# Kernel optimization log

Hardware: AMD Instinct MI355X
Metric: run time of the kernel (lower is better)

## Reference

```python
import jax, jax.numpy as jnp
import numpy as np

B, S, E, H, VS, VT = 128, 256, 512, 512, 32000, 32000


def _lstm_layer(x, mask, Wih, Whh, bih, bhh):
    # x: (S,B,E_in), mask: (S,B) bool. PyTorch gate order i,f,g,o.
    h0 = jnp.zeros((x.shape[1], Whh.shape[1]), x.dtype)
    c0 = h0
    def step(carry, inp):
        h, c = carry
        xt, mt = inp
        g = xt @ Wih.T + h @ Whh.T + bih + bhh
        i, f, gg, o = jnp.split(g, 4, axis=-1)
        i = jax.nn.sigmoid(i); f = jax.nn.sigmoid(f)
        gg = jnp.tanh(gg); o = jax.nn.sigmoid(o)
        c_new = f * c + i * gg
        h_new = o * jnp.tanh(c_new)
        m = mt[:, None]
        h2 = jnp.where(m, h_new, h)
        c2 = jnp.where(m, c_new, c)
        return (h2, c2), jnp.where(m, h_new, 0.0)  # pad_packed zero-pads
    (hT, cT), ys = jax.lax.scan(step, (h0, c0), (x, mask))
    return ys, cT


def setup_inputs() -> dict:
    key = jax.random.key(0)
    ks = jax.random.split(key, 32)
    def w(k, shape, fan_in):
        bound = 1.0 / np.sqrt(fan_in)
        return jax.random.uniform(k, shape, jnp.float32, -bound, bound)
    src_tokens = jax.random.randint(ks[0], (B, S), 0, VS)
    src_lens = jnp.sort(jax.random.randint(ks[1], (B,), S // 2, S + 1))[::-1]
    src_lens = src_lens.at[0].set(S)  # pack_padded expects descending, max = S
    trg_tokens = jax.random.randint(ks[2], (B,), 0, VT)
    inp = {
        'src_tokens': src_tokens, 'src_lens': src_lens, 'trg_tokens': trg_tokens,
        'src_emb': jax.random.normal(ks[3], (VS, E), jnp.float32),
        'trg_emb': jax.random.normal(ks[4], (VT, E), jnp.float32),
        'enc_Wih0': w(ks[5], (4 * H, E), H), 'enc_Whh0': w(ks[6], (4 * H, H), H),
        'enc_bih0': w(ks[7], (4 * H,), H), 'enc_bhh0': w(ks[8], (4 * H,), H),
        'enc_Wih1': w(ks[9], (4 * H, H), H), 'enc_Whh1': w(ks[10], (4 * H, H), H),
        'enc_bih1': w(ks[11], (4 * H,), H), 'enc_bhh1': w(ks[12], (4 * H,), H),
        'dec_Wih': w(ks[13], (4 * H, E + H), H), 'dec_Whh': w(ks[14], (4 * H, H), H),
        'dec_bih': w(ks[15], (4 * H,), H), 'dec_bhh': w(ks[16], (4 * H,), H),
        'W_init': w(ks[17], (H, 2 * H), 2 * H), 'b_init': w(ks[18], (H,), 2 * H),
        'W_hid': w(ks[19], (H, 2 * H), 2 * H), 'b_hid': w(ks[20], (H,), 2 * H),
        'W_out': w(ks[21], (VT, H), H), 'b_out': w(ks[22], (VT,), H),
    }
    return inp


def reference(src_tokens, src_lens, trg_tokens, src_emb, trg_emb,
              enc_Wih0, enc_Whh0, enc_bih0, enc_bhh0,
              enc_Wih1, enc_Whh1, enc_bih1, enc_bhh1,
              dec_Wih, dec_Whh, dec_bih, dec_bhh,
              W_init, b_init, W_hid, b_hid, W_out, b_out):
    # ---- encode ----
    x = src_emb[src_tokens]                       # (B,S,E)
    x = jnp.transpose(x, (1, 0, 2))               # (S,B,E)
    mask = jnp.arange(S)[:, None] < src_lens[None, :]  # (S,B)
    y0, c0f = _lstm_layer(x, mask, enc_Wih0, enc_Whh0, enc_bih0, enc_bhh0)
    y1, c1f = _lstm_layer(y0, mask, enc_Wih1, enc_Whh1, enc_bih1, enc_bhh1)
    src_states = jnp.transpose(y1, (1, 0, 2))     # (B,S,H)
    # final cell states (num_layers,B,H) -> (B, num_layers*H)
    final_cells = jnp.concatenate([c0f, c1f], axis=-1)  # (B,2H)
    c_dec = final_cells @ W_init.T + b_init       # (B,H)
    h_dec = jnp.tanh(c_dec)
    # ---- one decoder step ----
    emb_t = trg_emb[trg_tokens]                   # (B,E)
    vec = jnp.concatenate([emb_t, jnp.zeros((B, H), emb_t.dtype)], axis=-1)
    g = vec @ dec_Wih.T + h_dec @ dec_Whh.T + dec_bih + dec_bhh
    i, f, gg, o = jnp.split(g, 4, axis=-1)
    c = jax.nn.sigmoid(f) * c_dec + jax.nn.sigmoid(i) * jnp.tanh(gg)
    h = jax.nn.sigmoid(o) * jnp.tanh(c)           # (B,H)
    # ---- masked dot attention ----
    scores = jnp.einsum('bsh,bh->bs', src_states, h)
    smask = jnp.arange(S)[None, :] < src_lens[:, None]
    scores = jnp.where(smask, scores, -jnp.inf)
    attw = jax.nn.softmax(scores, axis=-1)
    context = jnp.einsum('bs,bsh->bh', attw, src_states)
    attn_vec = jnp.concatenate([h, context], axis=-1) @ W_hid.T + b_hid
    logits = attn_vec @ W_out.T + b_out
    prd_token = jnp.argmax(logits, axis=-1)       # softmax is monotone
    return context, h, prd_token
```

## Files before the change

### kernel.cpp

```cpp
#include <hip/hip_runtime.h>
#include <stdint.h>


typedef _Float16 f16;
typedef f16 f16x8 __attribute__((ext_vector_type(8)));
typedef float f32x4 __attribute__((ext_vector_type(4)));

#define LOSCALE 2048.0f
#define LOINV   (1.0f/2048.0f)

#define B_  128
#define S_  256
#define H_  512

__device__ __forceinline__ uint16_t hbits(f16 h){ union{ f16 f; uint16_t u; } c; c.f=h; return c.u; }

__device__ __forceinline__ uint32_t split_ph2(float x){
  f16 h = (f16)x;
  float r = (x - (float)h) * LOSCALE;
  return (uint32_t)hbits(h) | ((uint32_t)hbits((f16)r) << 16);
}
__device__ __forceinline__ float ph2val(uint32_t p){
  union{ uint16_t u; f16 f; } a, b; a.u = (uint16_t)p; b.u = (uint16_t)(p>>16);
  return (float)a.f + (float)b.f * LOINV;
}

__device__ __forceinline__ void pack_hi_lo(const uint4& a, const uint4& b, uint4& hi, uint4& lo){
  hi = make_uint4((a.x & 0xffffu) | (a.y << 16),
                  (a.z & 0xffffu) | (a.w << 16),
                  (b.x & 0xffffu) | (b.y << 16),
                  (b.z & 0xffffu) | (b.w << 16));
  lo = make_uint4((a.x >> 16) | (a.y & 0xffff0000u),
                  (a.z >> 16) | (a.w & 0xffff0000u),
                  (b.x >> 16) | (b.y & 0xffff0000u),
                  (b.z >> 16) | (b.w & 0xffff0000u));
}

__device__ __forceinline__ void split_pack8(const float* x, uint4& hi, uint4& lo){
  uint16_t h[8], l[8];
#pragma unroll
  for (int e = 0; e < 8; ++e) {
    f16 hh = (f16)x[e];
    float r = (x[e] - (float)hh) * LOSCALE;
    h[e] = hbits(hh); l[e] = hbits((f16)r);
  }
  hi = make_uint4((uint32_t)h[0]|((uint32_t)h[1]<<16), (uint32_t)h[2]|((uint32_t)h[3]<<16),
                  (uint32_t)h[4]|((uint32_t)h[5]<<16), (uint32_t)h[6]|((uint32_t)h[7]<<16));
  lo = make_uint4((uint32_t)l[0]|((uint32_t)l[1]<<16), (uint32_t)l[2]|((uint32_t)l[3]<<16),
                  (uint32_t)l[4]|((uint32_t)l[5]<<16), (uint32_t)l[6]|((uint32_t)l[7]<<16));
}

__device__ __forceinline__ f32x4 mfma16(uint4 a, uint4 b, f32x4 c){
  return __builtin_amdgcn_mfma_f32_16x16x32_f16(
      __builtin_bit_cast(f16x8, a), __builtin_bit_cast(f16x8, b), c, 0, 0, 0);
}

__device__ __forceinline__ float sigm(float x){ return 1.0f/(1.0f + expf(-x)); }
__device__ __forceinline__ float fsigm(float x){ return 1.0f/(1.0f + __expf(-x)); }
__device__ __forceinline__ float ftanh(float x){
  float ax = fabsf(x);
  float e = __expf(-2.0f*ax);
  float r = (1.0f - e)/(1.0f + e);
  return copysignf(r, x);
}

__device__ __forceinline__ uint32_t plane_word(uint32_t p, uint32_t pp, int odd){
  return odd ? ((pp >> 16) | (p & 0xffff0000u))
             : ((p & 0xffffu) | (pp << 16));
}

__device__ __forceinline__ size_t fl_idx(int row, int k){
  return (size_t)(k >> 5) * 4096 + (size_t)(row >> 4) * 512 + (size_t)(k & 1) * 256
       + (size_t)((k >> 3) & 3) * 64 + (size_t)(row & 15) * 4 + (size_t)((k & 7) >> 1);
}

__device__ __forceinline__ void gload_lds16(const uint32_t* gbase, uint32_t* lbase, int lane){
#if __has_builtin(__builtin_amdgcn_global_load_lds)
  __builtin_amdgcn_global_load_lds(
      (const __attribute__((address_space(1))) uint32_t*)(gbase + lane*4),
      (__attribute__((address_space(3))) uint32_t*)lbase, 16, 0, 0);
#else
  *(uint4*)(lbase + lane*4) = *(const uint4*)(gbase + lane*4);
#endif
}

__global__ __launch_bounds__(256) void k_embed_src_fl(const int* __restrict__ tok,
    const float* __restrict__ emb, uint32_t* __restrict__ out)
{
  const size_t total = (size_t)S_ * B_ * H_;
  for (size_t i = (size_t)blockIdx.x*256 + threadIdx.x; i < total; i += (size_t)gridDim.x*256) {
    int s = (int)(i >> 16), b = (int)((i >> 9) & 127), k = (int)(i & 511);
    int t = tok[b*S_ + s];
    uint32_t p = split_ph2(emb[(size_t)t*H_ + k]);
    uint32_t pp = __shfl_xor(p, 1);
    out[(size_t)s*65536 + fl_idx(b, k)] = plane_word(p, pp, k & 1);
  }
}

__global__ __launch_bounds__(256) void k_embed_trg(const int* __restrict__ tok,
    const float* __restrict__ emb, uint32_t* __restrict__ out)
{
  int i = blockIdx.x*256 + threadIdx.x;
  int e = i & (H_-1), b = i >> 9;
  int t = tok[b];
  out[i] = split_ph2(emb[(size_t)t*H_ + e]);
}

__global__ __launch_bounds__(256) void k_packW(const float* __restrict__ W,
    uint32_t* __restrict__ out)
{
  int i = blockIdx.x*256 + threadIdx.x;
  int n = i >> 9, k = i & 511;
  uint32_t p = split_ph2(W[i]);
  uint32_t pp = __shfl_xor(p, 1);
  out[(size_t)(n >> 7)*65536 + fl_idx(n & 127, k)] = plane_word(p, pp, k & 1);
}

__global__ __launch_bounds__(256) void k_packAfl(const float* __restrict__ a,
    uint32_t* __restrict__ out)
{
  int i = blockIdx.x*256 + threadIdx.x;
  int b = i >> 9, k = i & 511;
  uint32_t p = split_ph2(a[i]);
  uint32_t pp = __shfl_xor(p, 1);
  out[fl_idx(b, k)] = plane_word(p, pp, k & 1);
}

__global__ __launch_bounds__(256,2) void k_gemm_fl(
    const uint32_t* __restrict__ Afl,
    const uint32_t* __restrict__ Wfl,
    const float* __restrict__ b0, const float* __restrict__ b1,
    float* __restrict__ C, int N, int addC)
{
  __shared__ uint8_t sm[65536];
  const int tid = threadIdx.x, lane = tid & 63, wv = tid >> 6;
  const int wm = wv >> 1, wn = wv & 1;
  const int bn0 = blockIdx.x * 128, bm0 = blockIdx.y * 128;
  const uint32_t* Ab = Afl + (size_t)blockIdx.y * 65536;
  const uint32_t* Wb = Wfl + (size_t)blockIdx.x * 65536;

  f32x4 acc0[4][4], acc1[4][4];
#pragma unroll
  for (int i = 0; i < 4; ++i)
#pragma unroll
    for (int j = 0; j < 4; ++j) { acc0[i][j] = (f32x4){0,0,0,0}; acc1[i][j] = (f32x4){0,0,0,0}; }

  for (int it = 0; it < 8; ++it) {
    __syncthreads();
    {
      const uint32_t* gsrc = (wv < 2 ? Ab : Wb) + (size_t)it*8192 + (size_t)(wv & 1)*4096;
      uint32_t* lb = (uint32_t*)(sm + (size_t)wv*16384);
#pragma unroll
      for (int e = 0; e < 16; ++e)
        gload_lds16(gsrc + e*256, lb + e*256, lane);
    }
    asm volatile("s_waitcnt vmcnt(0)" ::: "memory");
    __syncthreads();

#pragma unroll
    for (int kt = 0; kt < 2; ++kt) {
      uint4 ah[4], al[4];
#pragma unroll
      for (int i = 0; i < 4; ++i) {
        const uint8_t* p = sm + (size_t)(kt*8 + wm*4 + i)*2048 + lane*16;
        ah[i] = *(const uint4*)p; al[i] = *(const uint4*)(p + 1024);
      }
#pragma unroll
      for (int j = 0; j < 4; ++j) {
        const uint8_t* p = sm + 32768 + (size_t)(kt*8 + wn*4 + j)*2048 + lane*16;
        uint4 bh = *(const uint4*)p;
        uint4 bl = *(const uint4*)(p + 1024);
#pragma unroll
        for (int i = 0; i < 4; ++i) {
          acc0[i][j] = mfma16(ah[i], bh, acc0[i][j]);
          acc1[i][j] = mfma16(al[i], bh, acc1[i][j]);
          acc1[i][j] = mfma16(ah[i], bl, acc1[i][j]);
        }
      }
    }
  }

#pragma unroll
  for (int i = 0; i < 4; ++i) {
    int row0 = bm0 + (wm*4+i)*16 + ((lane>>4)<<2);
#pragma unroll
    for (int j = 0; j < 4; ++j) {
      int col = bn0 + (wn*4+j)*16 + (lane & 15);
      float bias = 0.f;
      if (b0) bias += b0[col];
      if (b1) bias += b1[col];
      f32x4 v = acc0[i][j] + acc1[i][j] * LOINV;
#pragma unroll
      for (int r = 0; r < 4; ++r) {
        size_t idx = (size_t)(row0 + r) * N + col;
        float out = v[r] + bias;
        if (addC) out += C[idx];
        C[idx] = out;
      }
    }
  }
}

__global__ __launch_bounds__(256,2) void k_gemm(
    const uint32_t* __restrict__ A, int lda,
    const float* __restrict__ W, int ldw,
    const float* __restrict__ b0, const float* __restrict__ b1,
    float* __restrict__ C, int N, int K, int addC)
{
  __shared__ uint8_t sm[65536];
  const int tid = threadIdx.x;
  const int lane = tid & 63, wv = tid >> 6;
  const int wm = wv >> 1, wn = wv & 1;
  const int bn0 = blockIdx.x * 128, bm0 = blockIdx.y * 128;

  const int srow = tid >> 1;
  const int skh  = (tid & 1) * 32;
  const int smt  = srow >> 4, sr = srow & 15, skt = tid & 1;

  f32x4 acc0[4][4], acc1[4][4];
#pragma unroll
  for (int i = 0; i < 4; ++i)
#pragma unroll
    for (int j = 0; j < 4; ++j) { acc0[i][j] = (f32x4){0,0,0,0}; acc1[i][j] = (f32x4){0,0,0,0}; }

  for (int k0 = 0; k0 < K; k0 += 64) {
    __syncthreads();
    {
      const uint32_t* ap = A + (size_t)(bm0 + srow) * lda + (k0 + skh);
      uint4 q[8];
#pragma unroll
      for (int e = 0; e < 8; ++e) q[e] = *(const uint4*)(ap + e*4);
#pragma unroll
      for (int kg = 0; kg < 4; ++kg) {
        uint4 hi, lo; pack_hi_lo(q[2*kg], q[2*kg+1], hi, lo);
        uint8_t* dst = sm + (size_t)(smt*2 + skt)*2048 + (size_t)(sr + 16*kg)*16;
        *(uint4*)dst = hi; *(uint4*)(dst + 1024) = lo;
      }
    }
    {
      const float* wp = W + (size_t)(bn0 + srow) * ldw + (k0 + skh);
      float xs[32];
#pragma unroll
      for (int e = 0; e < 8; ++e) { float4 v = *(const float4*)(wp + e*4);
        xs[e*4+0]=v.x; xs[e*4+1]=v.y; xs[e*4+2]=v.z; xs[e*4+3]=v.w; }
#pragma unroll
      for (int kg = 0; kg < 4; ++kg) {
        uint4 hi, lo; split_pack8(xs + kg*8, hi, lo);
        uint8_t* dst = sm + 32768 + (size_t)(smt*2 + skt)*2048 + (size_t)(sr + 16*kg)*16;
        *(uint4*)dst = hi; *(uint4*)(dst + 1024) = lo;
      }
    }
    __syncthreads();

#pragma unroll
    for (int kt = 0; kt < 2; ++kt) {
      uint4 ah[4], al[4];
#pragma unroll
      for (int i = 0; i < 4; ++i) {
        const uint8_t* p = sm + (size_t)(((wm*4+i)*2 + kt))*2048 + lane*16;
        ah[i] = *(const uint4*)p; al[i] = *(const uint4*)(p + 1024);
      }
#pragma unroll
      for (int j = 0; j < 4; ++j) {
        const uint8_t* p = sm + 32768 + (size_t)(((wn*4+j)*2 + kt))*2048 + lane*16;
        uint4 bh = *(const uint4*)p;
        uint4 bl = *(const uint4*)(p + 1024);
#pragma unroll
        for (int i = 0; i < 4; ++i) {
          acc0[i][j] = mfma16(ah[i], bh, acc0[i][j]);
          acc1[i][j] = mfma16(al[i], bh, acc1[i][j]);
          acc1[i][j] = mfma16(ah[i], bl, acc1[i][j]);
        }
      }
    }
  }

#pragma unroll
  for (int i = 0; i < 4; ++i) {
    int row0 = bm0 + (wm*4+i)*16 + ((lane>>4)<<2);
#pragma unroll
    for (int j = 0; j < 4; ++j) {
      int col = bn0 + (wn*4+j)*16 + (lane & 15);
      float bias = 0.f;
      if (b0) bias += b0[col];
      if (b1) bias += b1[col];
      f32x4 v = acc0[i][j] + acc1[i][j] * LOINV;
#pragma unroll
      for (int r = 0; r < 4; ++r) {
        size_t idx = (size_t)(row0 + r) * N + col;
        float out = v[r] + bias;
        if (addC) out += C[idx];
        C[idx] = out;
      }
    }
  }
}

__global__ __launch_bounds__(256,1) void k_lstm2(
    const float* __restrict__ Whh0, const float* __restrict__ Whh1,
    const float* __restrict__ bih1, const float* __restrict__ bhh1,
    const float* __restrict__ xg,
    const int*  __restrict__ lens,
    uint32_t* __restrict__ mb0,
    uint32_t* __restrict__ mb1,
    float* __restrict__ cb0, float* __restrict__ cb1,
    uint32_t* __restrict__ y1buf,
    uint32_t* __restrict__ flg0, uint32_t* __restrict__ flg1,
    const uint32_t* __restrict__ Wp1,
    int s0, int nt)
{
  __shared__ uint8_t sm[163840];
  uint8_t* wih = sm;
  uint8_t* tile = sm + 131072;
  uint64_t* tile64 = (uint64_t*)tile;
  float* g0ex = (float*)tile;
  float* g1ex = (float*)(tile + 4096);

  const int tid = threadIdx.x, lane = tid & 63, wv = tid >> 6;
  const int bg = blockIdx.x & 7, hs = blockIdx.x >> 3;
  const int row = lane & 15, qh = lane >> 4;

  {
    const uint32_t* wpb = Wp1 + (size_t)(wv*4 + (hs >> 3))*65536 + (size_t)(hs & 7)*512;
    uint32_t* lb = (uint32_t*)(wih + (size_t)wv*32768);
#pragma unroll
    for (int kt = 0; kt < 16; ++kt) {
      gload_lds16(wpb + kt*4096,       lb + kt*512,       lane);
      gload_lds16(wpb + kt*4096 + 256, lb + kt*512 + 256, lane);
    }
  }

  uint4 w0h[16], w0l[16], w1h[16], w1l[16];
  {
    const float* r0 = Whh0 + (size_t)(wv*512 + hs*16 + row)*512 + qh*8;
    const float* r1 = Whh1 + (size_t)(wv*512 + hs*16 + row)*512 + qh*8;
#pragma unroll
    for (int kt = 0; kt < 16; ++kt) {
      float xs[8];
      float4 v0 = *(const float4*)(r0 + kt*32), v1 = *(const float4*)(r0 + kt*32 + 4);
      xs[0]=v0.x; xs[1]=v0.y; xs[2]=v0.z; xs[3]=v0.w;
      xs[4]=v1.x; xs[5]=v1.y; xs[6]=v1.z; xs[7]=v1.w;
      split_pack8(xs, w0h[kt], w0l[kt]);
      v0 = *(const float4*)(r1 + kt*32); v1 = *(const float4*)(r1 + kt*32 + 4);
      xs[0]=v0.x; xs[1]=v0.y; xs[2]=v0.z; xs[3]=v0.w;
      xs[4]=v1.x; xs[5]=v1.y; xs[6]=v1.z; xs[7]=v1.w;
      split_pack8(xs, w1h[kt], w1l[kt]);
    }
  }

  const int b_l = tid >> 4, uu = tid & 15;
  const int bglob = bg*16 + b_l;
  const size_t bgoff = (size_t)bg*8192;
  const int oct_p = hs*2 + (uu >> 3);
  const size_t widx = (size_t)b_l*512 + (size_t)(uu & 1)*256
                    + ((size_t)(oct_p ^ b_l) << 2) + (size_t)((uu & 7) >> 1);
  const int len_b = lens[bglob];
  const int lenA  = lens[bg*16 + row];
  float c0_reg = cb0[(size_t)bglob*512 + hs*16 + uu];
  float c1_reg = cb1[(size_t)bglob*512 + hs*16 + uu];
  float h0_reg, h1_reg;
  {
    size_t ib = (size_t)(s0 & 1)*65536 + bgoff + (size_t)b_l*512
              + ((size_t)(oct_p ^ b_l) << 2) + (size_t)((uu & 7) >> 1);
    uint32_t hiw = mb0[ib], low = mb0[ib + 256];
    int sh = (uu & 1) * 16;
    union{ uint16_t u; f16 f; } ch, cl;
    ch.u = (uint16_t)(hiw >> sh); cl.u = (uint16_t)(low >> sh);
    h0_reg = (float)ch.f + (float)cl.f * LOINV;
    int s1i = (s0 >= 1) ? (s0 - 1) : 0;
    size_t ib1 = (size_t)(s1i & 1)*65536 + bgoff + (size_t)b_l*512
               + ((size_t)(oct_p ^ b_l) << 2) + (size_t)((uu & 7) >> 1);
    hiw = mb1[ib1]; low = mb1[ib1 + 256];
    ch.u = (uint16_t)(hiw >> sh); cl.u = (uint16_t)(low >> sh);
    h1_reg = (float)ch.f + (float)cl.f * LOINV;
  }
  float b1g[4];
#pragma unroll
  for (int g = 0; g < 4; ++g)
    b1g[g] = bih1[g*512 + hs*16 + uu] + bhh1[g*512 + hs*16 + uu];
  const size_t yfl = (size_t)(hs >> 1)*4096 + (size_t)bg*512 + (size_t)(uu & 1)*256
                   + (size_t)((((hs & 1) << 1) | (uu >> 3)))*64 + (size_t)b_l*4
                   + (size_t)((uu & 7) >> 1);

  asm volatile("s_waitcnt vmcnt(0)" ::: "memory");
  __syncthreads();

  for (int it = 0; it < nt; ++it) {
    const int t = s0 + it;
    const bool aL0 = (t < 256);
    const bool aL1 = (t > 0);

    float xv0 = 0.f, xv1 = 0.f, xv2 = 0.f, xv3 = 0.f;
    if (aL0) {
      const float* xgp = xg + ((size_t)it*128 + bglob)*2048 + hs*16 + uu;
      xv0 = xgp[0]; xv1 = xgp[512]; xv2 = xgp[1024]; xv3 = xgp[1536];
    }

    if (it > 0) {
      if (wv == 0) {
        const uint32_t* fp = flg0 + bg*32 + (lane & 31);
        while (1) {
          uint32_t f = __hip_atomic_load(fp, __ATOMIC_RELAXED, __HIP_MEMORY_SCOPE_SYSTEM);
          if (__all((int)(f >= (uint32_t)t))) break;
          __builtin_amdgcn_s_sleep(1);
        }
      } else if (wv == 1) {
        const uint32_t* fp = flg1 + bg*32 + (lane & 31);
        while (1) {
          uint32_t f = __hip_atomic_load(fp, __ATOMIC_RELAXED, __HIP_MEMORY_SCOPE_SYSTEM);
          if (__all((int)(f >= (uint32_t)(t - 1)))) break;
          __builtin_amdgcn_s_sleep(1);
        }
      }
    }
    __builtin_amdgcn_s_barrier();
    __builtin_amdgcn_sched_barrier(0);

    const uint64_t* sp0 = (const uint64_t*)(mb0 + (size_t)(t & 1)*65536 + bgoff);
    const uint64_t* sp1 = (const uint64_t*)(mb1 + (size_t)((t - 1) & 1)*65536 + bgoff);
    uint64_t v0[16], v1[16];
#pragma unroll
    for (int e = 0; e < 16; ++e)
      v0[e] = __hip_atomic_load(sp0 + tid + e*256, __ATOMIC_RELAXED, __HIP_MEMORY_SCOPE_SYSTEM);
    if (aL1) {
#pragma unroll
      for (int e = 0; e < 16; ++e)
        v1[e] = __hip_atomic_load(sp1 + tid + e*256, __ATOMIC_RELAXED, __HIP_MEMORY_SCOPE_SYSTEM);
    }
#pragma unroll
    for (int e = 0; e < 16; ++e)
      tile64[tid + e*256] = v0[e];
    asm volatile("s_waitcnt lgkmcnt(0)" ::: "memory");
    __builtin_amdgcn_s_barrier();
    __builtin_amdgcn_sched_barrier(0);

    f32x4 A0 = (f32x4){0,0,0,0}, A1 = (f32x4){0,0,0,0}, A2 = (f32x4){0,0,0,0};
    f32x4 B0 = (f32x4){0,0,0,0}, B1 = (f32x4){0,0,0,0}, B2 = (f32x4){0,0,0,0};
    {
      const uint8_t* hrp = tile + (size_t)row*2048;
      const uint8_t* wbase = wih + (size_t)wv*32768;
      const bool cY = aL1 && ((t - 1) < lenA);
      const uint4 z4 = make_uint4(0,0,0,0);
#pragma unroll
      for (int kt = 0; kt < 16; ++kt) {
        int oct = kt*4 + qh;
        const uint8_t* pA = hrp + (((oct ^ row)) << 4);
        uint4 ah = *(const uint4*)pA, al = *(const uint4*)(pA + 1024);
        A0 = mfma16(ah, w0h[kt], A0);
        A1 = mfma16(al, w0h[kt], A1);
        A2 = mfma16(ah, w0l[kt], A2);
        uint4 yh = cY ? ah : z4, yl = cY ? al : z4;
        const uint8_t* pB = wbase + (size_t)kt*2048 + lane*16;
        uint4 bh = *(const uint4*)pB, bl = *(const uint4*)(pB + 1024);
        B0 = mfma16(yh, bh, B0);
        B1 = mfma16(yl, bh, B1);
        B2 = mfma16(yh, bl, B2);
      }
    }
    __builtin_amdgcn_sched_barrier(0);
    __builtin_amdgcn_s_barrier();
    __builtin_amdgcn_sched_barrier(0);

    if (aL1) {
#pragma unroll
      for (int e = 0; e < 16; ++e)
        tile64[tid + e*256] = v1[e];
    }
    asm volatile("s_waitcnt lgkmcnt(0)" ::: "memory");
    __builtin_amdgcn_s_barrier();
    __builtin_amdgcn_sched_barrier(0);

    if (aL1) {
      const uint8_t* hrp = tile + (size_t)row*2048;
#pragma unroll
      for (int kt = 0; kt < 16; ++kt) {
        int oct = kt*4 + qh;
        const uint8_t* pA = hrp + (((oct ^ row)) << 4);
        uint4 ah = *(const uint4*)pA, al = *(const uint4*)(pA + 1024);
        B0 = mfma16(ah, w1h[kt], B0);
        B1 = mfma16(al, w1h[kt], B1);
        B2 = mfma16(ah, w1l[kt], B2);
      }
    }
    __builtin_amdgcn_sched_barrier(0);
    __builtin_amdgcn_s_barrier();
    __builtin_amdgcn_sched_barrier(0);

    {
      int col = lane & 15, rb = (lane >> 4) << 2;
      if (aL0) {
#pragma unroll
        for (int r = 0; r < 4; ++r)
          g0ex[(size_t)(wv*16 + rb + r)*16 + col] = A0[r] + (A1[r] + A2[r])*LOINV;
      }
      if (aL1) {
#pragma unroll
        for (int r = 0; r < 4; ++r)
          g1ex[(size_t)(wv*16 + rb + r)*16 + col] = B0[r] + (B1[r] + B2[r])*LOINV;
      }
    }
    asm volatile("s_waitcnt lgkmcnt(0)" ::: "memory");
    __builtin_amdgcn_s_barrier();
    __builtin_amdgcn_sched_barrier(0);

    uint32_t p1w = 0; bool m1 = false;
    if (aL0) {
      float gi = g0ex[(size_t)(0*16 + b_l)*16 + uu] + xv0;
      float gf = g0ex[(size_t)(1*16 + b_l)*16 + uu] + xv1;
      float gg = g0ex[(size_t)(2*16 + b_l)*16 + uu] + xv2;
      float go = g0ex[(size_t)(3*16 + b_l)*16 + uu] + xv3;
      float cn = fsigm(gf)*c0_reg + fsigm(gi)*ftanh(gg);
      float hn = fsigm(go)*ftanh(cn);
      bool m = (t < len_b);
      c0_reg = m ? cn : c0_reg;
      h0_reg = m ? hn : h0_reg;
      uint32_t p = split_ph2(h0_reg);
      uint32_t pp = __shfl_xor(p, 1);
      __hip_atomic_store(mb0 + (size_t)((t + 1) & 1)*65536 + bgoff + widx,
                         plane_word(p, pp, uu & 1), __ATOMIC_RELAXED, __HIP_MEMORY_SCOPE_SYSTEM);
    }
    if (aL1) {
      float gi = g1ex[(size_t)(0*16 + b_l)*16 + uu] + b1g[0];
      float gf = g1ex[(size_t)(1*16 + b_l)*16 + uu] + b1g[1];
      float gg = g1ex[(size_t)(2*16 + b_l)*16 + uu] + b1g[2];
      float go = g1ex[(size_t)(3*16 + b_l)*16 + uu] + b1g[3];
      float cn = fsigm(gf)*c1_reg + fsigm(gi)*ftanh(gg);
      float hn = fsigm(go)*ftanh(cn);
      m1 = ((t - 1) < len_b);
      c1_reg = m1 ? cn : c1_reg;
      h1_reg = m1 ? hn : h1_reg;
      uint32_t p = split_ph2(h1_reg);
      uint32_t pp = __shfl_xor(p, 1);
      p1w = plane_word(p, pp, uu & 1);
      __hip_atomic_store(mb1 + (size_t)(t & 1)*65536 + bgoff + widx,
                         p1w, __ATOMIC_RELAXED, __HIP_MEMORY_SCOPE_SYSTEM);
    }
    asm volatile("s_waitcnt vmcnt(0)" ::: "memory");
    __builtin_amdgcn_s_barrier();
    __builtin_amdgcn_sched_barrier(0);
    if (tid == 0) {
      if (aL0) __hip_atomic_store(flg0 + bg*32 + hs, (uint32_t)(t + 1),
                                  __ATOMIC_RELAXED, __HIP_MEMORY_SCOPE_SYSTEM);
      if (aL1) __hip_atomic_store(flg1 + bg*32 + hs, (uint32_t)t,
                                  __ATOMIC_RELAXED, __HIP_MEMORY_SCOPE_SYSTEM);
    }
    if (aL1) y1buf[(size_t)(t - 1)*65536 + yfl] = m1 ? p1w : 0u;
  }
  cb0[(size_t)bglob*512 + hs*16 + uu] = c0_reg;
  cb1[(size_t)bglob*512 + hs*16 + uu] = c1_reg;
}

__global__ __launch_bounds__(256) void k_pack2(const float* __restrict__ a,
    const float* __restrict__ b, uint32_t* __restrict__ out)
{
  int i = blockIdx.x*256 + threadIdx.x;
  int bb = i >> 10, k = i & 1023;
  float x = (k < 512) ? a[(size_t)bb*512 + k] : b[(size_t)bb*512 + k - 512];
  out[i] = split_ph2(x);
}

__global__ __launch_bounds__(256) void k_tanh_split(const float* __restrict__ c,
    uint32_t* __restrict__ hp)
{ int i = blockIdx.x*256 + threadIdx.x; hp[i] = split_ph2(tanhf(c[i])); }

__global__ __launch_bounds__(256) void k_dec_cell(const float* __restrict__ g,
    const float* __restrict__ cdec, float* __restrict__ hout, float* __restrict__ dh)
{
  int i = blockIdx.x*256 + threadIdx.x;
  int b = i >> 9, u = i & 511;
  const float* gb = g + (size_t)b*2048;
  float c = sigm(gb[512 + u])*cdec[i] + sigm(gb[u])*tanhf(gb[1024 + u]);
  float h = sigm(gb[1536 + u])*tanhf(c);
  hout[i] = h; dh[i] = h;
}

__global__ __launch_bounds__(256) void k_attn(const uint32_t* __restrict__ y1,
    const float* __restrict__ h, const int* __restrict__ lens,
    float* __restrict__ ctx, float* __restrict__ dctx)
{
  __shared__ float hsh[512];
  __shared__ float sc[256];
  __shared__ float red[8];
  const int b = blockIdx.x, tid = threadIdx.x, lane = tid & 63, wv = tid >> 6;
  hsh[tid]       = h[(size_t)b*512 + tid];
  hsh[tid + 256] = h[(size_t)b*512 + tid + 256];
  const int len = lens[b];
  __syncthreads();

  const size_t lanebase = (size_t)(lane >> 2)*4096 + (size_t)(b >> 4)*512
                        + (size_t)(lane & 3)*64 + (size_t)(b & 15)*4;
  for (int it = 0; it < 64; ++it) {
    int s = wv*64 + it;
    const uint32_t* yb = y1 + (size_t)s*65536 + lanebase;
    uint4 hw = *(const uint4*)yb;
    uint4 lw = *(const uint4*)(yb + 256);
    int k0 = lane*8;
    uint32_t hws[4] = {hw.x,hw.y,hw.z,hw.w}, lws[4] = {lw.x,lw.y,lw.z,lw.w};
    float d = 0.f;
#pragma unroll
    for (int w = 0; w < 4; ++w) {
      union{uint16_t u; f16 f;} h0,h1,l0,l1;
      h0.u=(uint16_t)hws[w]; h1.u=(uint16_t)(hws[w]>>16);
      l0.u=(uint16_t)lws[w]; l1.u=(uint16_t)(lws[w]>>16);
      d += ((float)h0.f + (float)l0.f*LOINV) * hsh[k0 + 2*w]
         + ((float)h1.f + (float)l1.f*LOINV) * hsh[k0 + 2*w + 1];
    }
    for (int off = 32; off; off >>= 1) d += __shfl_xor(d, off);
    if (lane == 0) sc[s] = d;
  }
  __syncthreads();

  float v = (tid < len) ? sc[tid] : -INFINITY;
  float mx = v;
  for (int off = 32; off; off >>= 1) mx = fmaxf(mx, __shfl_xor(mx, off));
  if (lane == 0) red[wv] = mx;
  __syncthreads();
  mx = fmaxf(fmaxf(red[0], red[1]), fmaxf(red[2], red[3]));
  float e = (tid < len) ? expf(v - mx) : 0.f;
  float ssum = e;
  for (int off = 32; off; off >>= 1) ssum += __shfl_xor(ssum, off);
  if (lane == 0) red[4 + wv] = ssum;
  __syncthreads();
  float tot = red[4] + red[5] + red[6] + red[7];
  __syncthreads();
  sc[tid] = e / tot;
  __syncthreads();

  const int u0 = tid, u1 = tid + 256;
  const size_t bu0 = (size_t)(u0 >> 5)*4096 + (size_t)(b >> 4)*512
                   + (size_t)((u0 >> 3) & 3)*64 + (size_t)(b & 15)*4 + (size_t)((u0 & 7) >> 1);
  const size_t bu1 = (size_t)(u1 >> 5)*4096 + (size_t)(b >> 4)*512
                   + (size_t)((u1 >> 3) & 3)*64 + (size_t)(b & 15)*4 + (size_t)((u1 & 7) >> 1);
  const int sh = (tid & 1) * 16;
  float acc0 = 0.f, acc1 = 0.f;
  for (int s = 0; s < 256; ++s) {
    float w = sc[s];
    const uint32_t* yb = y1 + (size_t)s*65536;
    uint32_t hi0 = yb[bu0], lo0 = yb[bu0 + 256];
    uint32_t hi1 = yb[bu1], lo1 = yb[bu1 + 256];
    union{uint16_t u; f16 f;} a,b2,c2,d2;
    a.u =(uint16_t)(hi0 >> sh); b2.u=(uint16_t)(lo0 >> sh);
    c2.u=(uint16_t)(hi1 >> sh); d2.u=(uint16_t)(lo1 >> sh);
    acc0 += w*((float)a.f  + (float)b2.f*LOINV);
    acc1 += w*((float)c2.f + (float)d2.f*LOINV);
  }
  ctx [(size_t)b*512 + tid]       = acc0;  ctx [(size_t)b*512 + tid + 256] = acc1;
  dctx[(size_t)b*512 + tid]       = acc0;  dctx[(size_t)b*512 + tid + 256] = acc1;
}

__global__ __launch_bounds__(256) void k_argmax(const float* __restrict__ logits,
    float* __restrict__ out)
{
  __shared__ float bv[256];
  __shared__ int   bi[256];
  const int b = blockIdx.x, tid = threadIdx.x;
  const float* L = logits + (size_t)b*32000;
  float best = -INFINITY; int idx = 0;
  for (int i = tid; i < 32000; i += 256) {
    float v = L[i];
    if (v > best) { best = v; idx = i; }
  }
  bv[tid] = best; bi[tid] = idx;
  __syncthreads();
  for (int sft = 128; sft; sft >>= 1) {
    if (tid < sft) {
      if (bv[tid+sft] > bv[tid] || (bv[tid+sft] == bv[tid] && bi[tid+sft] < bi[tid])) {
        bv[tid] = bv[tid+sft]; bi[tid] = bi[tid+sft];
      }
    }
    __syncthreads();
  }
  if (tid == 0) out[b] = (float)bi[0];
}

extern "C" void kernel_launch(void* const* d_in, const int* in_sizes, int n_in,
                              void* d_out, int out_size, void* d_ws, size_t ws_size,
                              hipStream_t stream)
{
  (void)in_sizes; (void)n_in; (void)out_size; (void)ws_size;
  const int*   src_tokens = (const int*)  d_in[0];
  const int*   src_lens   = (const int*)  d_in[1];
  const int*   trg_tokens = (const int*)  d_in[2];
  const float* src_emb    = (const float*)d_in[3];
  const float* trg_emb    = (const float*)d_in[4];
  const float* Wih0 = (const float*)d_in[5];
  const float* Whh0 = (const float*)d_in[6];
  const float* bih0 = (const float*)d_in[7];
  const float* bhh0 = (const float*)d_in[8];
  const float* Wih1 = (const float*)d_in[9];
  const float* Whh1 = (const float*)d_in[10];
  const float* bih1 = (const float*)d_in[11];
  const float* bhh1 = (const float*)d_in[12];
  const float* dWih = (const float*)d_in[13];
  const float* dWhh = (const float*)d_in[14];
  const float* dbih = (const float*)d_in[15];
  const float* dbhh = (const float*)d_in[16];
  const float* Winit= (const float*)d_in[17];
  const float* binit= (const float*)d_in[18];
  const float* Whid = (const float*)d_in[19];
  const float* bhid = (const float*)d_in[20];
  const float* Wout = (const float*)d_in[21];
  const float* bout = (const float*)d_in[22];

  uint8_t* ws = (uint8_t*)d_ws;
  constexpr size_t MBs = 1ull << 20;
  constexpr size_t OFF_AP    = 0;
  constexpr size_t OFF_Y1    = 64*MBs;
  constexpr size_t OFF_XG    = 128*MBs;
  constexpr size_t OFF_MB    = 192*MBs;
  constexpr size_t OFF_CB0   = OFF_MB    + 1*MBs;
  constexpr size_t OFF_CB1   = OFF_CB0   + 256*1024;
  constexpr size_t OFF_FLG   = OFF_CB1   + 256*1024;
  constexpr size_t OFF_PK    = OFF_FLG   + 4096;
  constexpr size_t OFF_CDEC  = OFF_PK    + 512*1024;
  constexpr size_t OFF_HDECP = OFF_CDEC  + 256*1024;
  constexpr size_t OFF_EMBP  = OFF_HDECP + 256*1024;
  constexpr size_t OFF_G     = OFF_EMBP  + 256*1024;
  constexpr size_t OFF_HDEC2 = OFF_G     + 1*MBs;
  constexpr size_t OFF_CTX   = OFF_HDEC2 + 256*1024;
  constexpr size_t OFF_AVEC  = OFF_CTX   + 256*1024;
  constexpr size_t OFF_AVECP = OFF_AVEC  + 256*1024;
  constexpr size_t OFF_LOG   = OFF_AVECP + 256*1024;

  uint32_t* Ap    = (uint32_t*)(ws + OFF_AP);
  uint32_t* Y1    = (uint32_t*)(ws + OFF_Y1);
  float*    Xg    = (float*)   (ws + OFF_XG);
  uint32_t* WoutF = (uint32_t*)(ws + OFF_XG);
  uint32_t* mb0   = (uint32_t*)(ws + OFF_MB);
  uint32_t* mb1   = (uint32_t*)(ws + OFF_MB + 512*1024);
  float*    cb0   = (float*)   (ws + OFF_CB0);
  float*    cb1   = (float*)   (ws + OFF_CB1);
  uint32_t* flg0  = (uint32_t*)(ws + OFF_FLG);
  uint32_t* flg1  = (uint32_t*)(ws + OFF_FLG + 2048);
  uint32_t* pk    = (uint32_t*)(ws + OFF_PK);
  float*    cdec  = (float*)   (ws + OFF_CDEC);
  uint32_t* hdecp = (uint32_t*)(ws + OFF_HDECP);
  uint32_t* embp  = (uint32_t*)(ws + OFF_EMBP);
  float*    g     = (float*)   (ws + OFF_G);
  float*    hdec2 = (float*)   (ws + OFF_HDEC2);
  float*    ctx   = (float*)   (ws + OFF_CTX);
  float*    avec  = (float*)   (ws + OFF_AVEC);
  uint32_t* avecp = (uint32_t*)(ws + OFF_AVECP);
  float*    logit = (float*)   (ws + OFF_LOG);
  uint32_t* Wp0   = (uint32_t*)(ws + OFF_LOG);
  uint32_t* Wp1   = (uint32_t*)(ws + OFF_LOG + 4*MBs);
  float*    dout  = (float*)   d_out;

  k_packW<<<4096, 256, 0, stream>>>(Wih0, Wp0);
  k_packW<<<4096, 256, 0, stream>>>(Wih1, Wp1);

  hipMemsetAsync(mb0,  0, 1024*1024, stream);
  hipMemsetAsync(flg0, 0, 4096, stream);
  hipMemsetAsync(cb0,  0, 65536*4, stream);
  hipMemsetAsync(cb1,  0, 65536*4, stream);
  k_embed_src_fl<<<2048, 256, 0, stream>>>(src_tokens, src_emb, Ap);
  for (int c = 0; c < 4; ++c) {
    int s0 = c * 64;
    k_gemm_fl<<<dim3(16, 64), 256, 0, stream>>>(Ap + (size_t)s0*65536,
        Wp0, bih0, bhh0, Xg, 2048, 0);
    k_lstm2<<<256, 256, 0, stream>>>(Whh0, Whh1, bih1, bhh1, Xg, src_lens,
        mb0, mb1, cb0, cb1, Y1, flg0, flg1, Wp1, s0, (c == 3) ? 65 : 64);
  }

  k_packW<<<64000, 256, 0, stream>>>(Wout, WoutF);

  k_pack2<<<512, 256, 0, stream>>>(cb0, cb1, pk);
  k_gemm<<<dim3(4, 1), 256, 0, stream>>>(pk, 1024, Winit, 1024, binit, nullptr,
      cdec, 512, 1024, 0);
  k_tanh_split<<<256, 256, 0, stream>>>(cdec, hdecp);

  k_embed_trg<<<256, 256, 0, stream>>>(trg_tokens, trg_emb, embp);
  k_gemm<<<dim3(16, 1), 256, 0, stream>>>(embp, 512, dWih, 1024, dbih, dbhh,
      g, 2048, 512, 0);
  k_gemm<<<dim3(16, 1), 256, 0, stream>>>(hdecp, 512, dWhh, 512, nullptr, nullptr,
      g, 2048, 512, 1);
  k_dec_cell<<<256, 256, 0, stream>>>(g, cdec, hdec2, dout + 65536);

  k_attn<<<128, 256, 0, stream>>>(Y1, hdec2, src_lens, ctx, dout);

  k_pack2<<<512, 256, 0, stream>>>(hdec2, ctx, pk);
  k_gemm<<<dim3(4, 1), 256, 0, stream>>>(pk, 1024, Whid, 1024, bhid, nullptr,
      avec, 512, 1024, 0);
  k_packAfl<<<256, 256, 0, stream>>>(avec, avecp);
  k_gemm_fl<<<dim3(250, 1), 256, 0, stream>>>(avecp, WoutF, bout, nullptr,
      logit, 32000, 0);
  k_argmax<<<128, 256, 0, stream>>>(logit, dout + 131072);
}
```

Before: 2.484 ms.

## Split fused two-layer LSTM step into separately synchronized layer phases

```diff
diff --git a/kernel.cpp b/kernel.cpp
--- a/kernel.cpp
+++ b/kernel.cpp
@@ -396,47 +396,34 @@
       xv0 = xgp[0]; xv1 = xgp[512]; xv2 = xgp[1024]; xv3 = xgp[1536];
     }
 
-    if (it > 0) {
-      if (wv == 0) {
-        const uint32_t* fp = flg0 + bg*32 + (lane & 31);
-        while (1) {
-          uint32_t f = __hip_atomic_load(fp, __ATOMIC_RELAXED, __HIP_MEMORY_SCOPE_SYSTEM);
-          if (__all((int)(f >= (uint32_t)t))) break;
-          __builtin_amdgcn_s_sleep(1);
-        }
-      } else if (wv == 1) {
-        const uint32_t* fp = flg1 + bg*32 + (lane & 31);
-        while (1) {
-          uint32_t f = __hip_atomic_load(fp, __ATOMIC_RELAXED, __HIP_MEMORY_SCOPE_SYSTEM);
-          if (__all((int)(f >= (uint32_t)(t - 1)))) break;
-          __builtin_amdgcn_s_sleep(1);
-        }
-      }
-    }
-    __builtin_amdgcn_s_barrier();
-    __builtin_amdgcn_sched_barrier(0);
-
-    const uint64_t* sp0 = (const uint64_t*)(mb0 + (size_t)(t & 1)*65536 + bgoff);
-    const uint64_t* sp1 = (const uint64_t*)(mb1 + (size_t)((t - 1) & 1)*65536 + bgoff);
-    uint64_t v0[16], v1[16];
-#pragma unroll
-    for (int e = 0; e < 16; ++e)
-      v0[e] = __hip_atomic_load(sp0 + tid + e*256, __ATOMIC_RELAXED, __HIP_MEMORY_SCOPE_SYSTEM);
-    if (aL1) {
+    if (aL0 && it > 0 && wv == 0) {
+      const uint32_t* fp = flg0 + bg*32 + (lane & 31);
+      while (1) {
+        uint32_t f = __hip_atomic_load(fp, __ATOMIC_RELAXED, __HIP_MEMORY_SCOPE_SYSTEM);
+        if (__all((int)(f >= (uint32_t)t))) break;
+        __builtin_amdgcn_s_sleep(1);
+      }
+    }
+    __builtin_amdgcn_s_barrier();
+    __builtin_amdgcn_sched_barrier(0);
+
+    if (aL0) {
+      const uint64_t* sp0 = (const uint64_t*)(mb0 + (size_t)(t & 1)*65536 + bgoff);
+      uint64_t v0[16];
 #pragma unroll
       for (int e = 0; e < 16; ++e)
-        v1[e] = __hip_atomic_load(sp1 + tid + e*256, __ATOMIC_RELAXED, __HIP_MEMORY_SCOPE_SYSTEM);
-    }
-#pragma unroll
-    for (int e = 0; e < 16; ++e)
-      tile64[tid + e*256] = v0[e];
+        v0[e] = __hip_atomic_load(sp0 + tid + e*256, __ATOMIC_RELAXED, __HIP_MEMORY_SCOPE_SYSTEM);
+#pragma unroll
+      for (int e = 0; e < 16; ++e)
+        tile64[tid + e*256] = v0[e];
+    }
     asm volatile("s_waitcnt lgkmcnt(0)" ::: "memory");
     __builtin_amdgcn_s_barrier();
     __builtin_amdgcn_sched_barrier(0);
 
     f32x4 A0 = (f32x4){0,0,0,0}, A1 = (f32x4){0,0,0,0}, A2 = (f32x4){0,0,0,0};
     f32x4 B0 = (f32x4){0,0,0,0}, B1 = (f32x4){0,0,0,0}, B2 = (f32x4){0,0,0,0};
-    {
+    if (aL0) {
       const uint8_t* hrp = tile + (size_t)row*2048;
       const uint8_t* wbase = wih + (size_t)wv*32768;
       const bool cY = aL1 && ((t - 1) < lenA);
@@ -461,49 +448,16 @@
     __builtin_amdgcn_s_barrier();
     __builtin_amdgcn_sched_barrier(0);
 
-    if (aL1) {
-#pragma unroll
-      for (int e = 0; e < 16; ++e)
-        tile64[tid + e*256] = v1[e];
+    if (aL0) {
+      int col = lane & 15, rb = (lane >> 4) << 2;
+#pragma unroll
+      for (int r = 0; r < 4; ++r)
+        g0ex[(size_t)(wv*16 + rb + r)*16 + col] = A0[r] + (A1[r] + A2[r])*LOINV;
     }
     asm volatile("s_waitcnt lgkmcnt(0)" ::: "memory");
     __builtin_amdgcn_s_barrier();
     __builtin_amdgcn_sched_barrier(0);
 
-    if (aL1) {
-      const uint8_t* hrp = tile + (size_t)row*2048;
-#pragma unroll
-      for (int kt = 0; kt < 16; ++kt) {
-        int oct = kt*4 + qh;
-        const uint8_t* pA = hrp + (((oct ^ row)) << 4);
-        uint4 ah = *(const uint4*)pA, al = *(const uint4*)(pA + 1024);
-        B0 = mfma16(ah, w1h[kt], B0);
-        B1 = mfma16(al, w1h[kt], B1);
-        B2 = mfma16(ah, w1l[kt], B2);
-      }
-    }
-    __builtin_amdgcn_sched_barrier(0);
-    __builtin_amdgcn_s_barrier();
-    __builtin_amdgcn_sched_barrier(0);
-
-    {
-      int col = lane & 15, rb = (lane >> 4) << 2;
-      if (aL0) {
-#pragma unroll
-        for (int r = 0; r < 4; ++r)
-          g0ex[(size_t)(wv*16 + rb + r)*16 + col] = A0[r] + (A1[r] + A2[r])*LOINV;
-      }
-      if (aL1) {
-#pragma unroll
-        for (int r = 0; r < 4; ++r)
-          g1ex[(size_t)(wv*16 + rb + r)*16 + col] = B0[r] + (B1[r] + B2[r])*LOINV;
-      }
-    }
-    asm volatile("s_waitcnt lgkmcnt(0)" ::: "memory");
-    __builtin_amdgcn_s_barrier();
-    __builtin_amdgcn_sched_barrier(0);
-
-    uint32_t p1w = 0; bool m1 = false;
     if (aL0) {
       float gi = g0ex[(size_t)(0*16 + b_l)*16 + uu] + xv0;
       float gf = g0ex[(size_t)(1*16 + b_l)*16 + uu] + xv1;
@@ -519,6 +473,65 @@
       __hip_atomic_store(mb0 + (size_t)((t + 1) & 1)*65536 + bgoff + widx,
                          plane_word(p, pp, uu & 1), __ATOMIC_RELAXED, __HIP_MEMORY_SCOPE_SYSTEM);
     }
+    asm volatile("s_waitcnt vmcnt(0)" ::: "memory");
+    __builtin_amdgcn_s_barrier();
+    __builtin_amdgcn_sched_barrier(0);
+    if (tid == 0 && aL0)
+      __hip_atomic_store(flg0 + bg*32 + hs, (uint32_t)(t + 1),
+                         __ATOMIC_RELAXED, __HIP_MEMORY_SCOPE_SYSTEM);
+
+    if (aL1 && it > 0 && wv == 0) {
+      const uint32_t* fp = flg1 + bg*32 + (lane & 31);
+      while (1) {
+        uint32_t f = __hip_atomic_load(fp, __ATOMIC_RELAXED, __HIP_MEMORY_SCOPE_SYSTEM);
+        if (__all((int)(f >= (uint32_t)(t - 1)))) break;
+        __builtin_amdgcn_s_sleep(1);
+      }
+    }
+    __builtin_amdgcn_s_barrier();
+    __builtin_amdgcn_sched_barrier(0);
+
+    if (aL1) {
+      const uint64_t* sp1 = (const uint64_t*)(mb1 + (size_t)((t - 1) & 1)*65536 + bgoff);
+      uint64_t v1[16];
+#pragma unroll
+      for (int e = 0; e < 16; ++e)
+        v1[e] = __hip_atomic_load(sp1 + tid + e*256, __ATOMIC_RELAXED, __HIP_MEMORY_SCOPE_SYSTEM);
+#pragma unroll
+      for (int e = 0; e < 16; ++e)
+        tile64[tid + e*256] = v1[e];
+    }
+    asm volatile("s_waitcnt lgkmcnt(0)" ::: "memory");
+    __builtin_amdgcn_s_barrier();
+    __builtin_amdgcn_sched_barrier(0);
+
+    if (aL1) {
+      const uint8_t* hrp = tile + (size_t)row*2048;
+#pragma unroll
+      for (int kt = 0; kt < 16; ++kt) {
+        int oct = kt*4 + qh;
+        const uint8_t* pA = hrp + (((oct ^ row)) << 4);
+        uint4 ah = *(const uint4*)pA, al = *(const uint4*)(pA + 1024);
+        B0 = mfma16(ah, w1h[kt], B0);
+        B1 = mfma16(al, w1h[kt], B1);
+        B2 = mfma16(ah, w1l[kt], B2);
+      }
+    }
+    __builtin_amdgcn_sched_barrier(0);
+    __builtin_amdgcn_s_barrier();
+    __builtin_amdgcn_sched_barrier(0);
+
+    if (aL1) {
+      int col = lane & 15, rb = (lane >> 4) << 2;
+#pragma unroll
+      for (int r = 0; r < 4; ++r)
+        g1ex[(size_t)(wv*16 + rb + r)*16 + col] = B0[r] + (B1[r] + B2[r])*LOINV;
+    }
+    asm volatile("s_waitcnt lgkmcnt(0)" ::: "memory");
+    __builtin_amdgcn_s_barrier();
+    __builtin_amdgcn_sched_barrier(0);
+
+    uint32_t p1w = 0; bool m1 = false;
     if (aL1) {
       float gi = g1ex[(size_t)(0*16 + b_l)*16 + uu] + b1g[0];
       float gf = g1ex[(size_t)(1*16 + b_l)*16 + uu] + b1g[1];
@@ -538,12 +551,9 @@
     asm volatile("s_waitcnt vmcnt(0)" ::: "memory");
     __builtin_amdgcn_s_barrier();
     __builtin_amdgcn_sched_barrier(0);
-    if (tid == 0) {
-      if (aL0) __hip_atomic_store(flg0 + bg*32 + hs, (uint32_t)(t + 1),
-                                  __ATOMIC_RELAXED, __HIP_MEMORY_SCOPE_SYSTEM);
-      if (aL1) __hip_atomic_store(flg1 + bg*32 + hs, (uint32_t)t,
-                                  __ATOMIC_RELAXED, __HIP_MEMORY_SCOPE_SYSTEM);
-    }
+    if (tid == 0 && aL1)
+      __hip_atomic_store(flg1 + bg*32 + hs, (uint32_t)t,
+                         __ATOMIC_RELAXED, __HIP_MEMORY_SCOPE_SYSTEM);
     if (aL1) y1buf[(size_t)(t - 1)*65536 + yfl] = m1 ? p1w : 0u;
   }
   cb0[(size_t)bglob*512 + hs*16 + uu] = c0_reg;
```

After: 2.545 ms. 1.02x slower.

## Map LSTM batch groups to XCDs and relax atomics to agent scope

Applied to the files above, without the earlier changes.

```diff
diff --git a/kernel.cpp b/kernel.cpp
--- a/kernel.cpp
+++ b/kernel.cpp
@@ -306,6 +306,7 @@
     float* __restrict__ cb0, float* __restrict__ cb1,
     uint32_t* __restrict__ y1buf,
     uint32_t* __restrict__ flg0, uint32_t* __restrict__ flg1,
+    uint32_t* __restrict__ xcdclaim,
     const uint32_t* __restrict__ Wp1,
     int s0, int nt)
 {
@@ -317,8 +318,21 @@
   float* g1ex = (float*)(tile + 4096);
 
   const int tid = threadIdx.x, lane = tid & 63, wv = tid >> 6;
-  const int bg = blockIdx.x & 7, hs = blockIdx.x >> 3;
   const int row = lane & 15, qh = lane >> 4;
+
+  uint32_t* claim_sh = (uint32_t*)tile;
+  if (tid == 0) {
+    uint32_t xcd;
+    asm volatile("s_getreg_b32 %0, hwreg(HW_REG_XCC_ID)" : "=s"(xcd));
+    xcd &= 7u;
+    uint32_t pos = __hip_atomic_fetch_add(xcdclaim + xcd*16, 1u,
+                     __ATOMIC_RELAXED, __HIP_MEMORY_SCOPE_SYSTEM);
+    claim_sh[0] = xcd | ((pos & 31u) << 8);
+  }
+  __syncthreads();
+  const uint32_t cl = claim_sh[0];
+  const int bg = (int)(cl & 7u), hs = (int)((cl >> 8) & 31u);
+  __syncthreads();
 
   {
     const uint32_t* wpb = Wp1 + (size_t)(wv*4 + (hs >> 3))*65536 + (size_t)(hs & 7)*512;
@@ -364,15 +378,15 @@
               + ((size_t)(oct_p ^ b_l) << 2) + (size_t)((uu & 7) >> 1);
     uint32_t hiw = mb0[ib], low = mb0[ib + 256];
     int sh = (uu & 1) * 16;
-    union{ uint16_t u; f16 f; } ch, cl;
-    ch.u = (uint16_t)(hiw >> sh); cl.u = (uint16_t)(low >> sh);
-    h0_reg = (float)ch.f + (float)cl.f * LOINV;
+    union{ uint16_t u; f16 f; } ch, cl2;
+    ch.u = (uint16_t)(hiw >> sh); cl2.u = (uint16_t)(low >> sh);
+    h0_reg = (float)ch.f + (float)cl2.f * LOINV;
     int s1i = (s0 >= 1) ? (s0 - 1) : 0;
     size_t ib1 = (size_t)(s1i & 1)*65536 + bgoff + (size_t)b_l*512
                + ((size_t)(oct_p ^ b_l) << 2) + (size_t)((uu & 7) >> 1);
     hiw = mb1[ib1]; low = mb1[ib1 + 256];
-    ch.u = (uint16_t)(hiw >> sh); cl.u = (uint16_t)(low >> sh);
-    h1_reg = (float)ch.f + (float)cl.f * LOINV;
+    ch.u = (uint16_t)(hiw >> sh); cl2.u = (uint16_t)(low >> sh);
+    h1_reg = (float)ch.f + (float)cl2.f * LOINV;
   }
   float b1g[4];
 #pragma unroll
@@ -400,14 +414,14 @@
       if (wv == 0) {
         const uint32_t* fp = flg0 + bg*32 + (lane & 31);
         while (1) {
-          uint32_t f = __hip_atomic_load(fp, __ATOMIC_RELAXED, __HIP_MEMORY_SCOPE_SYSTEM);
+          uint32_t f = __hip_atomic_load(fp, __ATOMIC_RELAXED, __HIP_MEMORY_SCOPE_AGENT);
           if (__all((int)(f >= (uint32_t)t))) break;
           __builtin_amdgcn_s_sleep(1);
         }
       } else if (wv == 1) {
         const uint32_t* fp = flg1 + bg*32 + (lane & 31);
         while (1) {
-          uint32_t f = __hip_atomic_load(fp, __ATOMIC_RELAXED, __HIP_MEMORY_SCOPE_SYSTEM);
+          uint32_t f = __hip_atomic_load(fp, __ATOMIC_RELAXED, __HIP_MEMORY_SCOPE_AGENT);
           if (__all((int)(f >= (uint32_t)(t - 1)))) break;
           __builtin_amdgcn_s_sleep(1);
         }
@@ -421,11 +435,11 @@
     uint64_t v0[16], v1[16];
 #pragma unroll
     for (int e = 0; e < 16; ++e)
-      v0[e] = __hip_atomic_load(sp0 + tid + e*256, __ATOMIC_RELAXED, __HIP_MEMORY_SCOPE_SYSTEM);
+      v0[e] = __hip_atomic_load(sp0 + tid + e*256, __ATOMIC_RELAXED, __HIP_MEMORY_SCOPE_AGENT);
     if (aL1) {
 #pragma unroll
       for (int e = 0; e < 16; ++e)
-        v1[e] = __hip_atomic_load(sp1 + tid + e*256, __ATOMIC_RELAXED, __HIP_MEMORY_SCOPE_SYSTEM);
+        v1[e] = __hip_atomic_load(sp1 + tid + e*256, __ATOMIC_RELAXED, __HIP_MEMORY_SCOPE_AGENT);
     }
 #pragma unroll
     for (int e = 0; e < 16; ++e)
@@ -517,7 +531,7 @@
       uint32_t p = split_ph2(h0_reg);
       uint32_t pp = __shfl_xor(p, 1);
       __hip_atomic_store(mb0 + (size_t)((t + 1) & 1)*65536 + bgoff + widx,
-                         plane_word(p, pp, uu & 1), __ATOMIC_RELAXED, __HIP_MEMORY_SCOPE_SYSTEM);
+                         plane_word(p, pp, uu & 1), __ATOMIC_RELAXED, __HIP_MEMORY_SCOPE_AGENT);
     }
     if (aL1) {
       float gi = g1ex[(size_t)(0*16 + b_l)*16 + uu] + b1g[0];
@@ -533,16 +547,16 @@
       uint32_t pp = __shfl_xor(p, 1);
       p1w = plane_word(p, pp, uu & 1);
       __hip_atomic_store(mb1 + (size_t)(t & 1)*65536 + bgoff + widx,
-                         p1w, __ATOMIC_RELAXED, __HIP_MEMORY_SCOPE_SYSTEM);
+                         p1w, __ATOMIC_RELAXED, __HIP_MEMORY_SCOPE_AGENT);
     }
     asm volatile("s_waitcnt vmcnt(0)" ::: "memory");
     __builtin_amdgcn_s_barrier();
     __builtin_amdgcn_sched_barrier(0);
     if (tid == 0) {
       if (aL0) __hip_atomic_store(flg0 + bg*32 + hs, (uint32_t)(t + 1),
-                                  __ATOMIC_RELAXED, __HIP_MEMORY_SCOPE_SYSTEM);
+                                  __ATOMIC_RELAXED, __HIP_MEMORY_SCOPE_AGENT);
       if (aL1) __hip_atomic_store(flg1 + bg*32 + hs, (uint32_t)t,
-                                  __ATOMIC_RELAXED, __HIP_MEMORY_SCOPE_SYSTEM);
+                                  __ATOMIC_RELAXED, __HIP_MEMORY_SCOPE_AGENT);
     }
     if (aL1) y1buf[(size_t)(t - 1)*65536 + yfl] = m1 ? p1w : 0u;
   }
@@ -731,6 +745,7 @@
   float*    cb0   = (float*)   (ws + OFF_CB0);
   float*    cb1   = (float*)   (ws + OFF_CB1);
   uint32_t* flg0  = (uint32_t*)(ws + OFF_FLG);
+  uint32_t* xclm  = (uint32_t*)(ws + OFF_FLG + 1024);
   uint32_t* flg1  = (uint32_t*)(ws + OFF_FLG + 2048);
   uint32_t* pk    = (uint32_t*)(ws + OFF_PK);
   float*    cdec  = (float*)   (ws + OFF_CDEC);
@@ -759,7 +774,7 @@
     k_gemm_fl<<<dim3(16, 64), 256, 0, stream>>>(Ap + (size_t)s0*65536,
         Wp0, bih0, bhh0, Xg, 2048, 0);
     k_lstm2<<<256, 256, 0, stream>>>(Whh0, Whh1, bih1, bhh1, Xg, src_lens,
-        mb0, mb1, cb0, cb1, Y1, flg0, flg1, Wp1, s0, (c == 3) ? 65 : 64);
+        mb0, mb1, cb0, cb1, Y1, flg0, flg1, xclm, Wp1, s0, (c == 3) ? 65 : 64);
   }
 
   k_packW<<<64000, 256, 0, stream>>>(Wout, WoutF);
```

Result: no change. 2.501 ms (+0.7%).
